# Kernel optimization log

Hardware: AMD Instinct MI355X
Metric: run time of the kernel (lower is better)

The kernel has to match this reference:

```python
import jax, jax.numpy as jnp
import numpy as np

HEADS = 16
EPS = 1e-6


def setup_inputs() -> dict:
    key = jax.random.key(0)
    k1, k2, k3 = jax.random.split(key, 3)
    B, N, C = 4, 4096, 1024
    x = jax.random.normal(k1, (B, N, C), dtype=jnp.float32)
    w_qkv = jax.random.normal(k2, (3 * C, C), dtype=jnp.float32) * (C ** -0.5)
    w_out = jax.random.normal(k3, (C, C), dtype=jnp.float32) * (C ** -0.5)
    b_out = jnp.zeros((C,), dtype=jnp.float32)
    return {"x": x, "w_qkv": w_qkv, "w_out": w_out, "b_out": b_out}


def reference(x, w_qkv, w_out, b_out):
    B, N, C = x.shape
    H = HEADS
    D = C // H
    scale = D ** -0.25

    qkv = x @ w_qkv.T  # [B, N, 3C]
    q, k, v = jnp.split(qkv, 3, axis=-1)

    def heads(t):  # [B, N, C] -> [B, H, N, D]
        return t.reshape(B, N, H, D).transpose(0, 2, 1, 3)

    q, k, v = heads(q), heads(k), heads(v)

    feat = lambda t: jax.nn.elu(t) + 1.0
    q = feat(q) * scale
    k = feat(k) * scale

    kv = jnp.einsum('bhnd,bhne->bhde', k, v)      # [B, H, D, D]
    out = jnp.einsum('bhnd,bhde->bhne', q, kv)    # [B, H, N, D]
    k_sum = k.sum(axis=2)                          # [B, H, D]
    denom = jnp.einsum('bhnd,bhd->bhn', q, k_sum)  # [B, H, N]
    out = out / (denom[..., None] + EPS)

    out = out.transpose(0, 2, 1, 3).reshape(B, N, C)
    return out @ w_out.T + b_out
```

## Files before the change

kernel.cpp:

```cpp
#include <hip/hip_runtime.h>
#include <hip/hip_bf16.h>
#include <cmath>


typedef __bf16 bf16_t;
typedef __attribute__((ext_vector_type(8))) __bf16 bf16x8;
typedef __attribute__((ext_vector_type(4))) __bf16 bf16x4;
typedef __attribute__((ext_vector_type(4))) float f32x4;
typedef __attribute__((ext_vector_type(8))) float f32x8;

#define MFMA16(a, b, c) __builtin_amdgcn_mfma_f32_16x16x32_bf16((a), (b), (c), 0, 0, 0)

#define LDS_PITCH 72

__device__ __forceinline__ f32x4 zf4() { f32x4 z; z[0] = 0.f; z[1] = 0.f; z[2] = 0.f; z[3] = 0.f; return z; }

__device__ __forceinline__ float feat(float x) { return x > 0.f ? x + 1.f : expf(x); }

__device__ __forceinline__ void gld_lds16(const bf16_t* src, bf16_t* dst)
{
    __builtin_amdgcn_global_load_lds(
        (__attribute__((address_space(1))) void*)const_cast<bf16_t*>(src),
        (__attribute__((address_space(3))) void*)dst, 16, 0, 0);
}

template <int NR>
__device__ __forceinline__ void stage_async(const bf16_t* g, int ld, bf16_t* lds, int tid)
{
    const int w = tid >> 6, l = tid & 63;
    constexpr int CALLS = NR >> 5;
#pragma unroll
    for (int p = 0; p < CALLS; ++p) {
        const int chunk = w * CALLS + p;
        const int gidx = chunk * 64 + l;
        const int row = gidx >> 3;
        const int cp = gidx & 7;
        const int c = cp ^ (row & 7);
        gld_lds16(g + row * ld + c * 8, lds + chunk * 512);
    }
}

__device__ __forceinline__ bf16x8 read_frag_sw(const bf16_t* lds, int row, int cg)
{
    const int sw = cg ^ (row & 7);
    return *(const bf16x8*)(lds + row * 64 + sw * 8);
}

__global__ __launch_bounds__(256) void cvt3_kernel(
    const float* __restrict__ x, bf16_t* __restrict__ xb,
    const float* __restrict__ wq, bf16_t* __restrict__ wqb,
    const float* __restrict__ wo, bf16_t* __restrict__ wob)
{
    const int bid = blockIdx.x;
    const float* src;
    bf16_t* dst;
    int base;
    if (bid < 8192)      { src = x;  dst = xb;  base = bid; }
    else if (bid < 9728) { src = wq; dst = wqb; base = bid - 8192; }
    else                 { src = wo; dst = wob; base = bid - 9728; }
    const size_t idx = ((size_t)base * 256 + threadIdx.x) * 8;
    f32x8 f = *(const f32x8*)(src + idx);
    bf16x8 v;
#pragma unroll
    for (int t = 0; t < 8; ++t) v[t] = (bf16_t)f[t];
    *(bf16x8*)(dst + idx) = v;
}

template <int MODE>
__global__ __launch_bounds__(256, 4) void gemm_bt_kernel(
    const bf16_t* __restrict__ A, const bf16_t* __restrict__ B, int K,
    void* __restrict__ out0, bf16_t* __restrict__ out1, bf16_t* __restrict__ out2,
    const float* __restrict__ bias)
{
    __shared__ __align__(16) bf16_t As[128 * 64];
    __shared__ __align__(16) bf16_t Bs[128 * 64];
    const int tid = threadIdx.x;
    const int l = tid & 63, w = tid >> 6;
    const int wm = w >> 1, wn = w & 1;
    const int quad = l >> 4, r16 = l & 15;
    const int m0 = blockIdx.y * 128;
    const int n0 = blockIdx.x * 128;

    f32x4 acc[4][4];
#pragma unroll
    for (int i = 0; i < 4; ++i)
#pragma unroll
        for (int j = 0; j < 4; ++j) acc[i][j] = zf4();

    const bf16_t* Ab = A + (size_t)m0 * K;
    const bf16_t* Bb = B + (size_t)n0 * K;

    for (int k0 = 0; k0 < K; k0 += 64) {
        stage_async<128>(Ab + k0, K, As, tid);
        stage_async<128>(Bb + k0, K, Bs, tid);
        __syncthreads();
#pragma unroll
        for (int ks = 0; ks < 2; ++ks) {
            const int cg = ks * 4 + quad;
            bf16x8 af[4], bfr[4];
#pragma unroll
            for (int i = 0; i < 4; ++i) af[i] = read_frag_sw(As, wm * 64 + i * 16 + r16, cg);
#pragma unroll
            for (int j = 0; j < 4; ++j) bfr[j] = read_frag_sw(Bs, wn * 64 + j * 16 + r16, cg);
#pragma unroll
            for (int i = 0; i < 4; ++i)
#pragma unroll
                for (int j = 0; j < 4; ++j)
                    acc[i][j] = MFMA16(af[i], bfr[j], acc[i][j]);
        }
        __syncthreads();
    }

    const float scale = 0.3535533905932738f;
#pragma unroll
    for (int i = 0; i < 4; ++i) {
        const int mbase = m0 + wm * 64 + i * 16 + quad * 4;
#pragma unroll
        for (int j = 0; j < 4; ++j) {
            const int col = n0 + wn * 64 + j * 16 + r16;
            if (MODE == 1) {
                float* yp = (float*)out0;
                const float bb = bias[col];
#pragma unroll
                for (int r = 0; r < 4; ++r)
                    yp[(size_t)(mbase + r) * 1024 + col] = acc[i][j][r] + bb;
            } else {
                const int part = col >> 10;
                const int cc = col & 1023;
                const int hh = (mbase >> 12) * 16 + (cc >> 6);
                const int d = cc & 63;
                const int ntok = mbase & 4095;
                if (part == 0) {
                    bf16_t* qp = (bf16_t*)out0 + ((size_t)hh * 4096 + ntok) * 64 + d;
#pragma unroll
                    for (int r = 0; r < 4; ++r)
                        qp[(size_t)r * 64] = (bf16_t)(feat(acc[i][j][r]) * scale);
                } else {
                    bf16_t* tp = (part == 1 ? out1 : out2) + ((size_t)hh * 64 + d) * 4096 + ntok;
                    bf16x4 pk;
#pragma unroll
                    for (int r = 0; r < 4; ++r) {
                        float v = acc[i][j][r];
                        if (part == 1) v = feat(v) * scale;
                        pk[r] = (bf16_t)v;
                    }
                    *(bf16x4*)tp = pk;
                }
            }
        }
    }
}

__global__ __launch_bounds__(256, 2) void kv_partial_kernel(
    const bf16_t* __restrict__ KT, const bf16_t* __restrict__ VT,
    float* __restrict__ kvp, float* __restrict__ ksp_out)
{
    __shared__ __align__(16) bf16_t Ks[64 * 64];
    __shared__ __align__(16) bf16_t Vs[64 * 64];
    const int tid = threadIdx.x;
    const int l = tid & 63, w = tid >> 6;
    const int quad = l >> 4, r16 = l & 15;
    const int hh = blockIdx.x;
    const int ksp = blockIdx.y;
    const bf16_t* kb = KT + (size_t)hh * 64 * 4096 + ksp * 512;
    const bf16_t* vb = VT + (size_t)hh * 64 * 4096 + ksp * 512;

    bf16x8 ones;
#pragma unroll
    for (int t = 0; t < 8; ++t) ones[t] = (bf16_t)1.0f;

    f32x4 acc[4], accks[4];
#pragma unroll
    for (int j = 0; j < 4; ++j) { acc[j] = zf4(); accks[j] = zf4(); }

    for (int k0 = 0; k0 < 512; k0 += 64) {
        stage_async<64>(kb + k0, 4096, Ks, tid);
        stage_async<64>(vb + k0, 4096, Vs, tid);
        __syncthreads();
#pragma unroll
        for (int ks = 0; ks < 2; ++ks) {
            const int cg = ks * 4 + quad;
            bf16x8 af = read_frag_sw(Vs, w * 16 + r16, cg);
            bf16x8 bk[4];
#pragma unroll
            for (int j = 0; j < 4; ++j) bk[j] = read_frag_sw(Ks, j * 16 + r16, cg);
#pragma unroll
            for (int j = 0; j < 4; ++j) acc[j] = MFMA16(af, bk[j], acc[j]);
            if (w == 0) {
#pragma unroll
                for (int j = 0; j < 4; ++j) accks[j] = MFMA16(ones, bk[j], accks[j]);
            }
        }
        __syncthreads();
    }

    float* ob = kvp + (size_t)(hh * 8 + ksp) * 4096;
    const int ebase = w * 16 + quad * 4;
#pragma unroll
    for (int j = 0; j < 4; ++j)
#pragma unroll
        for (int r = 0; r < 4; ++r)
            ob[(ebase + r) * 64 + j * 16 + r16] = acc[j][r];

    if (w == 0 && quad == 0) {
        float* kso = ksp_out + (size_t)(hh * 8 + ksp) * 64;
#pragma unroll
        for (int j = 0; j < 4; ++j) kso[j * 16 + r16] = accks[j][0];
    }
}

__global__ __launch_bounds__(256, 2) void attn_out_kernel(
    const bf16_t* __restrict__ Q, const float* __restrict__ kvp, const float* __restrict__ ksp,
    bf16_t* __restrict__ att)
{
    __shared__ __align__(16) bf16_t kvT[64 * LDS_PITCH];
    __shared__ __align__(16) bf16_t ksb[64];
    const int tid = threadIdx.x;
    const int l = tid & 63, w = tid >> 6;
    const int quad = l >> 4, r16 = l & 15;
    const int hh = blockIdx.x;
    const int b = hh >> 4, h = hh & 15;
    const int mt = blockIdx.y;

    {
        const int e = tid >> 2, d0 = (tid & 3) * 16;
        const float* kvph = kvp + (size_t)hh * 8 * 4096 + e * 64 + d0;
        f32x4 s[4];
#pragma unroll
        for (int q4 = 0; q4 < 4; ++q4) s[q4] = *(const f32x4*)(kvph + q4 * 4);
#pragma unroll
        for (int p = 1; p < 8; ++p)
#pragma unroll
            for (int q4 = 0; q4 < 4; ++q4) s[q4] += *(const f32x4*)(kvph + p * 4096 + q4 * 4);
        bf16x8 o0, o1;
#pragma unroll
        for (int r = 0; r < 4; ++r) {
            o0[r] = (bf16_t)s[0][r]; o0[4 + r] = (bf16_t)s[1][r];
            o1[r] = (bf16_t)s[2][r]; o1[4 + r] = (bf16_t)s[3][r];
        }
        *(bf16x8*)(kvT + e * LDS_PITCH + d0)     = o0;
        *(bf16x8*)(kvT + e * LDS_PITCH + d0 + 8) = o1;
        if (tid < 64) {
            const float* kp = ksp + (size_t)hh * 8 * 64 + tid;
            float ks = 0.f;
#pragma unroll
            for (int p = 0; p < 8; ++p) ks += kp[p * 64];
            ksb[tid] = (bf16_t)ks;
        }
    }
    __syncthreads();

    f32x4 acc[4][4];
    f32x4 dacc[4];
#pragma unroll
    for (int i = 0; i < 4; ++i) {
        dacc[i] = zf4();
#pragma unroll
        for (int j = 0; j < 4; ++j) acc[i][j] = zf4();
    }

    const int m0w = mt * 256 + w * 64;
    const bf16_t* qb = Q + (size_t)hh * 4096 * 64;
#pragma unroll
    for (int ks = 0; ks < 2; ++ks) {
        bf16x8 kf = *(const bf16x8*)(ksb + ks * 32 + quad * 8);
        if (r16 != 0) {
#pragma unroll
            for (int t = 0; t < 8; ++t) kf[t] = (bf16_t)0.f;
        }
        bf16x8 bfr[4];
#pragma unroll
        for (int j = 0; j < 4; ++j)
            bfr[j] = *(const bf16x8*)(kvT + (j * 16 + r16) * LDS_PITCH + ks * 32 + quad * 8);
#pragma unroll
        for (int i = 0; i < 4; ++i) {
            const bf16_t* qp = qb + (size_t)(m0w + i * 16 + r16) * 64 + ks * 32 + quad * 8;
            const bf16x8 af = *(const bf16x8*)qp;
            dacc[i] = MFMA16(af, kf, dacc[i]);
#pragma unroll
            for (int j = 0; j < 4; ++j) acc[i][j] = MFMA16(af, bfr[j], acc[i][j]);
        }
    }

#pragma unroll
    for (int i = 0; i < 4; ++i) {
        float den[4];
#pragma unroll
        for (int r = 0; r < 4; ++r)
            den[r] = __shfl(dacc[i][r], l & 48) + 1e-6f;
#pragma unroll
        for (int j = 0; j < 4; ++j) {
            const size_t colb = (size_t)h * 64 + j * 16 + r16;
#pragma unroll
            for (int r = 0; r < 4; ++r) {
                const int ntok = m0w + i * 16 + quad * 4 + r;
                att[((size_t)b * 4096 + ntok) * 1024 + colb] = (bf16_t)(acc[i][j][r] / den[r]);
            }
        }
    }
}

extern "C" void kernel_launch(void* const* d_in, const int* in_sizes, int n_in,
                              void* d_out, int out_size, void* d_ws, size_t ws_size,
                              hipStream_t stream)
{
    const float* x    = (const float*)d_in[0];
    const float* wqkv = (const float*)d_in[1];
    const float* wout = (const float*)d_in[2];
    const float* bout = (const float*)d_in[3];
    float* y = (float*)d_out;

    char* ws = (char*)d_ws;
    bf16_t* xb    = (bf16_t*)ws;
    bf16_t* wqkvb = (bf16_t*)(ws + (size_t)32 * 1048576);
    bf16_t* woutb = (bf16_t*)(ws + (size_t)38 * 1048576);
    bf16_t* Q     = (bf16_t*)(ws + (size_t)40 * 1048576);
    bf16_t* KT    = (bf16_t*)(ws + (size_t)72 * 1048576);
    bf16_t* VT    = (bf16_t*)(ws + (size_t)104 * 1048576);
    float* kvp    = (float*)ws;
    float* ksp    = (float*)(ws + (size_t)8 * 1048576);
    bf16_t* att   = KT;

    cvt3_kernel<<<10240, 256, 0, stream>>>(x, xb, wqkv, wqkvb, wout, woutb);

    gemm_bt_kernel<0><<<dim3(24, 128), 256, 0, stream>>>(xb, wqkvb, 1024, Q, KT, VT, nullptr);
    kv_partial_kernel<<<dim3(64, 8), 256, 0, stream>>>(KT, VT, kvp, ksp);
    attn_out_kernel<<<dim3(64, 16), 256, 0, stream>>>(Q, kvp, ksp, att);
    gemm_bt_kernel<1><<<dim3(8, 128), 256, 0, stream>>>(att, woutb, 1024, y, nullptr, nullptr, bout);
}
```

Before: 331.4 us.

## Swizzle GEMM blocks across XCDs and load kv partials directly from global

The GEMM kernel remaps block IDs so that consecutive tiles are grouped per XCD (bid mod 8), with the aim of better L2 locality for shared A/B tiles. The kv_partial kernel drops LDS staging and barriers, reads MFMA fragments straight from global memory, and doubles the sequence split to 16 chunks for more parallelism. In exchange, the attention-output kernel must reduce twice as many fp32 partials, and the workspace offset for ksp moves. Uncoalesced direct global fragment loads may cost bandwidth.

```diff
diff --git a/kernel.cpp b/kernel.cpp
--- a/kernel.cpp
+++ b/kernel.cpp
@@ -78,8 +78,13 @@
     const int l = tid & 63, w = tid >> 6;
     const int wm = w >> 1, wn = w & 1;
     const int quad = l >> 4, r16 = l & 15;
-    const int m0 = blockIdx.y * 128;
-    const int n0 = blockIdx.x * 128;
+
+    const int nwg = gridDim.x * gridDim.y;
+    const int cpx = nwg >> 3;
+    const int bid = blockIdx.y * gridDim.x + blockIdx.x;
+    const int swz = (bid & 7) * cpx + (bid >> 3);
+    const int m0 = (swz / gridDim.x) * 128;
+    const int n0 = (swz % gridDim.x) * 128;
 
     f32x4 acc[4][4];
 #pragma unroll
@@ -151,19 +156,18 @@
     }
 }
 
-__global__ __launch_bounds__(256, 2) void kv_partial_kernel(
+__global__ __launch_bounds__(256) void kv_partial_kernel(
     const bf16_t* __restrict__ KT, const bf16_t* __restrict__ VT,
     float* __restrict__ kvp, float* __restrict__ ksp_out)
 {
-    __shared__ __align__(16) bf16_t Ks[64 * 64];
-    __shared__ __align__(16) bf16_t Vs[64 * 64];
     const int tid = threadIdx.x;
     const int l = tid & 63, w = tid >> 6;
     const int quad = l >> 4, r16 = l & 15;
     const int hh = blockIdx.x;
     const int ksp = blockIdx.y;
-    const bf16_t* kb = KT + (size_t)hh * 64 * 4096 + ksp * 512;
-    const bf16_t* vb = VT + (size_t)hh * 64 * 4096 + ksp * 512;
+    const bf16_t* kb = KT + (size_t)hh * 64 * 4096 + ksp * 256 + quad * 8;
+    const bf16_t* vb = VT + (size_t)hh * 64 * 4096 + ksp * 256 + quad * 8;
+    const bf16_t* vrow = vb + (size_t)(w * 16 + r16) * 4096;
 
     bf16x8 ones;
 #pragma unroll
@@ -173,28 +177,23 @@
 #pragma unroll
     for (int j = 0; j < 4; ++j) { acc[j] = zf4(); accks[j] = zf4(); }
 
-    for (int k0 = 0; k0 < 512; k0 += 64) {
-        stage_async<64>(kb + k0, 4096, Ks, tid);
-        stage_async<64>(vb + k0, 4096, Vs, tid);
-        __syncthreads();
-#pragma unroll
-        for (int ks = 0; ks < 2; ++ks) {
-            const int cg = ks * 4 + quad;
-            bf16x8 af = read_frag_sw(Vs, w * 16 + r16, cg);
-            bf16x8 bk[4];
-#pragma unroll
-            for (int j = 0; j < 4; ++j) bk[j] = read_frag_sw(Ks, j * 16 + r16, cg);
-#pragma unroll
-            for (int j = 0; j < 4; ++j) acc[j] = MFMA16(af, bk[j], acc[j]);
-            if (w == 0) {
-#pragma unroll
-                for (int j = 0; j < 4; ++j) accks[j] = MFMA16(ones, bk[j], accks[j]);
-            }
-        }
-        __syncthreads();
-    }
-
-    float* ob = kvp + (size_t)(hh * 8 + ksp) * 4096;
+#pragma unroll
+    for (int kk = 0; kk < 8; ++kk) {
+        const int off = kk * 32;
+        const bf16x8 af = *(const bf16x8*)(vrow + off);
+        bf16x8 bk[4];
+#pragma unroll
+        for (int j = 0; j < 4; ++j)
+            bk[j] = *(const bf16x8*)(kb + (size_t)(j * 16 + r16) * 4096 + off);
+#pragma unroll
+        for (int j = 0; j < 4; ++j) acc[j] = MFMA16(af, bk[j], acc[j]);
+        if (w == 0) {
+#pragma unroll
+            for (int j = 0; j < 4; ++j) accks[j] = MFMA16(ones, bk[j], accks[j]);
+        }
+    }
+
+    float* ob = kvp + (size_t)(hh * 16 + ksp) * 4096;
     const int ebase = w * 16 + quad * 4;
 #pragma unroll
     for (int j = 0; j < 4; ++j)
@@ -203,7 +202,7 @@
             ob[(ebase + r) * 64 + j * 16 + r16] = acc[j][r];
 
     if (w == 0 && quad == 0) {
-        float* kso = ksp_out + (size_t)(hh * 8 + ksp) * 64;
+        float* kso = ksp_out + (size_t)(hh * 16 + ksp) * 64;
 #pragma unroll
         for (int j = 0; j < 4; ++j) kso[j * 16 + r16] = accks[j][0];
     }
@@ -224,12 +223,12 @@
 
     {
         const int e = tid >> 2, d0 = (tid & 3) * 16;
-        const float* kvph = kvp + (size_t)hh * 8 * 4096 + e * 64 + d0;
+        const float* kvph = kvp + (size_t)hh * 16 * 4096 + e * 64 + d0;
         f32x4 s[4];
 #pragma unroll
         for (int q4 = 0; q4 < 4; ++q4) s[q4] = *(const f32x4*)(kvph + q4 * 4);
 #pragma unroll
-        for (int p = 1; p < 8; ++p)
+        for (int p = 1; p < 16; ++p)
 #pragma unroll
             for (int q4 = 0; q4 < 4; ++q4) s[q4] += *(const f32x4*)(kvph + p * 4096 + q4 * 4);
         bf16x8 o0, o1;
@@ -241,10 +240,10 @@
         *(bf16x8*)(kvT + e * LDS_PITCH + d0)     = o0;
         *(bf16x8*)(kvT + e * LDS_PITCH + d0 + 8) = o1;
         if (tid < 64) {
-            const float* kp = ksp + (size_t)hh * 8 * 64 + tid;
+            const float* kp = ksp + (size_t)hh * 16 * 64 + tid;
             float ks = 0.f;
 #pragma unroll
-            for (int p = 0; p < 8; ++p) ks += kp[p * 64];
+            for (int p = 0; p < 16; ++p) ks += kp[p * 64];
             ksb[tid] = (bf16_t)ks;
         }
     }
@@ -318,13 +317,13 @@
     bf16_t* KT    = (bf16_t*)(ws + (size_t)72 * 1048576);
     bf16_t* VT    = (bf16_t*)(ws + (size_t)104 * 1048576);
     float* kvp    = (float*)ws;
-    float* ksp    = (float*)(ws + (size_t)8 * 1048576);
+    float* ksp    = (float*)(ws + (size_t)16 * 1048576);
     bf16_t* att   = KT;
 
     cvt3_kernel<<<10240, 256, 0, stream>>>(x, xb, wqkv, wqkvb, wout, woutb);
 
     gemm_bt_kernel<0><<<dim3(24, 128), 256, 0, stream>>>(xb, wqkvb, 1024, Q, KT, VT, nullptr);
-    kv_partial_kernel<<<dim3(64, 8), 256, 0, stream>>>(KT, VT, kvp, ksp);
+    kv_partial_kernel<<<dim3(64, 16), 256, 0, stream>>>(KT, VT, kvp, ksp);
     attn_out_kernel<<<dim3(64, 16), 256, 0, stream>>>(Q, kvp, ksp, att);
     gemm_bt_kernel<1><<<dim3(8, 128), 256, 0, stream>>>(att, woutb, 1024, y, nullptr, nullptr, bout);
 }
```

Result: no change. 336.3 us (+1.4%).
